# Optimization experiments

Measured on AMD Instinct MI355X. Metric: run time of the kernel, lower is better.

The kernel has to match this reference:

```python
import jax, jax.numpy as jnp
import numpy as np
import math

HIDDEN = 256
NUM_GAUSSIANS = 64
NUM_FILTERS = 256
CUTOFF = 1.0
COSINE_OFFSET = 0.0
N_NODES = 10000
N_EDGES = 320000


def ssp(x):
    # shifted softplus: softplus(x) - log(2)
    return jax.nn.softplus(x) - jnp.log(2.0).astype(x.dtype)


def setup_inputs() -> dict:
    key = jax.random.key(0)
    ks = jax.random.split(key, 12)

    def xavier(k, fan_out, fan_in):
        a = math.sqrt(6.0 / (fan_in + fan_out))
        return jax.random.uniform(k, (fan_out, fan_in), jnp.float32, -a, a)

    x = jax.random.normal(ks[0], (N_NODES, HIDDEN), jnp.float32)
    ji_pairs = jax.random.randint(ks[1], (2, N_EDGES), 0, N_NODES, jnp.int64)
    e_ji = jax.random.uniform(ks[2], (N_EDGES,), jnp.float32)  # distances in [0, cutoff)
    e_ji_basis = jax.random.normal(ks[3], (N_EDGES, NUM_GAUSSIANS), jnp.float32)

    return {
        "x": x,
        "ji_pairs": ji_pairs,
        "e_ji": e_ji,
        "e_ji_basis": e_ji_basis,
        # filter_nn: Linear(G->F), ssp, Linear(F->F)
        "fw1": xavier(ks[4], NUM_FILTERS, NUM_GAUSSIANS),
        "fb1": jnp.zeros((NUM_FILTERS,), jnp.float32),
        "fw2": xavier(ks[5], NUM_FILTERS, NUM_FILTERS),
        "fb2": jnp.zeros((NUM_FILTERS,), jnp.float32),
        # CFConv linears
        "w1": xavier(ks[6], NUM_FILTERS, HIDDEN),            # linear1, no bias
        "w2": xavier(ks[7], HIDDEN, NUM_FILTERS),            # linear2
        "b2": jnp.zeros((HIDDEN,), jnp.float32),
        # linear3
        "w3": xavier(ks[8], HIDDEN, HIDDEN),
        "b3": jnp.zeros((HIDDEN,), jnp.float32),
    }


def reference(x, ji_pairs, e_ji, e_ji_basis, fw1, fb1, fw2, fb2, w1, w2, b2, w3, b3):
    pi = jnp.asarray(math.pi, x.dtype)
    # cosine cutoff: C = 0.25 * (cos((e - off) * pi / (cutoff - off)) + 1)
    C = 0.25 * (jnp.cos((e_ji - COSINE_OFFSET) * pi / (CUTOFF - COSINE_OFFSET)) + 1.0)
    # filter network on edge RBF features: [E, F]
    W = ssp(e_ji_basis @ fw1.T + fb1) @ fw2.T + fb2
    W = W * C[:, None]
    # linear1 (no bias): [N, F]
    h = x @ w1.T
    # message: x_j * W, gathered from source nodes ji_pairs[0]
    src, dst = ji_pairs[0], ji_pairs[1]
    msg = h[src] * W                                   # [E, F]
    agg = jax.ops.segment_sum(msg, dst, num_segments=x.shape[0])  # [N, F]
    # linear2
    out = agg @ w2.T + b2
    # interaction block tail: act + linear3
    out = ssp(out) @ w3.T + b3
    return out
```

## Files before the change

### kernel.cpp

```cpp
#include <hip/hip_runtime.h>
#include <hip/hip_bf16.h>

typedef __bf16 bf16_t;
typedef float f32x4 __attribute__((ext_vector_type(4)));
typedef __bf16 bf16x8 __attribute__((ext_vector_type(8)));

#define NNODES 10000
#define NEDGES 320000
#define NPAD   10048
#define NB2    (NEDGES / 64)

#define OFF_AGG   256
#define OFF_JIN   (OFF_AGG  + (size_t)NPAD * 256 * 4)
#define OFF_HIST  (OFF_JIN  + (size_t)2 * NEDGES * 4)
#define OFF_CUR   (OFF_HIST + 10240 * 4)
#define OFF_CSR   (OFF_CUR  + 10240 * 4)
#define OFF_PERM  (OFF_CSR  + 10240 * 4)
#define OFF_SRCS  (OFF_PERM + (size_t)NEDGES * 4)
#define OFF_DSTS  (OFF_SRCS + (size_t)NEDGES * 4)
#define OFF_CES   (OFF_DSTS + (size_t)NEDGES * 4)
#define OFF_CE    (OFF_CES  + (size_t)NEDGES * 4)
#define OFF_WB    (OFF_CE   + (size_t)NEDGES * 4)
#define FW1B 0
#define FW2B 16384
#define W1B  81920
#define W2B  147456
#define W3B  212992
#define FB1B 278528
#define FB2B 278784
#define B2B  279040
#define B3B  279296
#define WBN  279552
#define WS_NEED (OFF_WB + (size_t)WBN * 2)

__device__ __forceinline__ float ssp_f(float v) {
    return fmaxf(v, 0.f) + __logf(1.f + __expf(-fabsf(v))) - 0.69314718055994531f;
}
__device__ __forceinline__ f32x4 mfma16(bf16x8 a, bf16x8 b, f32x4 c) {
    return __builtin_amdgcn_mfma_f32_16x16x32_bf16(a, b, c, 0, 0, 0);
}
template<bool ISB>
__device__ __forceinline__ bf16x8 ld8(const void* p, size_t off) {
    if constexpr (ISB) return *(const bf16x8*)((const bf16_t*)p + off);
    else {
        const float* f = (const float*)p + off;
        f32x4 lo = *(const f32x4*)f, hi = *(const f32x4*)(f + 4);
        bf16x8 r;
        for (int j = 0; j < 4; ++j) { r[j] = (bf16_t)lo[j]; r[j + 4] = (bf16_t)hi[j]; }
        return r;
    }
}
template<bool ISB>
__device__ __forceinline__ void st1(void* p, size_t off, float v) {
    if constexpr (ISB) ((bf16_t*)p)[off] = (bf16_t)v;
    else               ((float*)p)[off] = v;
}
__device__ __forceinline__ float ld1r(bool isb, const void* p, size_t off) {
    return isb ? (float)((const bf16_t*)p)[off] : ((const float*)p)[off];
}

__global__ __launch_bounds__(256) void detect_kernel(
    const void* __restrict__ x, const int* __restrict__ jraw,
    int* __restrict__ flags, int* __restrict__ hist)
{
    __shared__ int cnt, hi;
    if (threadIdx.x == 0) { cnt = 0; hi = 0; }
    __syncthreads();
    const unsigned short* xw = (const unsigned short*)x;
    int local = 0;
    for (int i = threadIdx.x; i < 2048; i += 256) {
        unsigned int e = (xw[2 * i] >> 7) & 0xFF;
        if (e >= 100 && e <= 141) local++;
    }
    atomicAdd(&cnt, local);
    int v = 0;
    for (int i = threadIdx.x; i < 1024; i += 256) v |= jraw[2 * i + 1];
    if (v != 0) atomicOr(&hi, 1);
    for (int i = threadIdx.x; i < 10240; i += 256) hist[i] = 0;
    __syncthreads();
    if (threadIdx.x == 0) { flags[0] = (cnt > 1024) ? 1 : 0; flags[1] = (hi == 0) ? 1 : 0; }
}

__global__ __launch_bounds__(256) void prep_kernel(
    const int* __restrict__ raw, const int* __restrict__ flags,
    const void* __restrict__ e_ji,
    const void* fw1, const void* fb1, const void* fw2, const void* fb2,
    const void* w1, const void* w2, const void* b2, const void* w3, const void* b3,
    int* __restrict__ jin, int* __restrict__ hist, float* __restrict__ ce,
    bf16_t* __restrict__ wb, float* __restrict__ agg)
{
    const bool is64 = (flags[1] != 0);
    const bool isb  = (flags[0] != 0);
    const int gid = blockIdx.x * 256 + threadIdx.x;
    if (gid < 2 * NEDGES) {
        int iv = is64 ? raw[2 * gid] : raw[gid];
        iv = iv < 0 ? 0 : (iv >= NNODES ? NNODES - 1 : iv);
        jin[gid] = iv;
        if (gid >= NEDGES) atomicAdd(&hist[iv], 1);
    }
    if (gid < NEDGES)
        ce[gid] = 0.25f * (cosf(3.14159265358979f * ld1r(isb, e_ji, gid)) + 1.0f);
    if (gid < WBN) {
        int g = gid; const void* s; int so;
        if      (g < FW2B) { s = fw1; so = g - FW1B; }
        else if (g < W1B)  { s = fw2; so = g - FW2B; }
        else if (g < W2B)  { s = w1;  so = g - W1B; }
        else if (g < W3B)  { s = w2;  so = g - W2B; }
        else if (g < FB1B) { s = w3;  so = g - W3B; }
        else if (g < FB2B) { s = fb1; so = g - FB1B; }
        else if (g < B2B)  { s = fb2; so = g - FB2B; }
        else if (g < B3B)  { s = b2;  so = g - B2B; }
        else               { s = b3;  so = g - B3B; }
        wb[gid] = (bf16_t)ld1r(isb, s, so);
    }
    f32x4 z = {0.f, 0.f, 0.f, 0.f};
    for (int i = gid; i < NPAD * 256 / 4; i += 2500 * 256)
        ((f32x4*)agg)[i] = z;
}

__global__ __launch_bounds__(256) void scan_kernel(
    const int* __restrict__ hist, int* __restrict__ cur, int* __restrict__ csr)
{
    __shared__ int s[256];
    const int t = threadIdx.x;
    int loc[40]; int sum = 0;
    const int base = t * 40;
    for (int j = 0; j < 40; ++j) {
        int i = base + j;
        loc[j] = (i < NNODES) ? hist[i] : 0;
        sum += loc[j];
    }
    s[t] = sum; __syncthreads();
    for (int off = 1; off < 256; off <<= 1) {
        int v = (t >= off) ? s[t - off] : 0;
        __syncthreads();
        if (t >= off) s[t] += v;
        __syncthreads();
    }
    int pre = (t == 0) ? 0 : s[t - 1];
    for (int j = 0; j < 40; ++j) {
        int i = base + j;
        cur[i] = pre;
        csr[i] = pre;
        pre += loc[j];
    }
}

__global__ __launch_bounds__(256) void scatter_kernel(
    const int* __restrict__ jin, const float* __restrict__ ce,
    int* __restrict__ cur, int* __restrict__ perm,
    int* __restrict__ src_s, int* __restrict__ dst_s, float* __restrict__ ce_s)
{
    int e = blockIdx.x * 256 + threadIdx.x;
    if (e < NEDGES) {
        int d = jin[NEDGES + e];
        int pos = atomicAdd(&cur[d], 1);
        perm[pos]  = e;
        src_s[pos] = jin[e];
        dst_s[pos] = d;
        ce_s[pos]  = ce[e];
    }
}

template<bool ISB>
__global__ __launch_bounds__(256, 2) void h_gemm_kernel(
    const void* __restrict__ x, const bf16_t* __restrict__ wb,
    bf16_t* __restrict__ h, const int* __restrict__ flags)
{
    if ((flags[0] != 0) != ISB) return;
    const bf16_t* w1b = wb + W1B;
    const int w = threadIdx.x >> 6, L = threadIdx.x & 63;
    const int lane16 = L & 15, quad = L >> 4;
    const int nb = blockIdx.x * 64, cb = w * 64;
    f32x4 acc[4][4] = {};
    for (int kc = 0; kc < 8; ++kc) {
        const int ko = kc * 32 + quad * 8;
        bf16x8 af[4], bfr[4];
        for (int mt = 0; mt < 4; ++mt) {
            int row = nb + mt * 16 + lane16;
            if (row >= NNODES) row = NNODES - 1;
            af[mt] = ld8<ISB>(x, (size_t)row * 256 + ko);
        }
        for (int nt = 0; nt < 4; ++nt)
            bfr[nt] = *(const bf16x8*)(w1b + (size_t)(cb + nt * 16 + lane16) * 256 + ko);
        for (int mt = 0; mt < 4; ++mt)
            for (int nt = 0; nt < 4; ++nt)
                acc[mt][nt] = mfma16(af[mt], bfr[nt], acc[mt][nt]);
    }
    for (int mt = 0; mt < 4; ++mt)
        for (int r = 0; r < 4; ++r) {
            int row = nb + mt * 16 + quad * 4 + r;
            if (row < NNODES)
                for (int nt = 0; nt < 4; ++nt)
                    h[(size_t)row * 256 + cb + nt * 16 + lane16] = (bf16_t)acc[mt][nt][r];
        }
}

template<bool ISB>
__global__ __launch_bounds__(256, 4) void edge_kernel2(
    const void* __restrict__ basis, const int* __restrict__ perm,
    const int* __restrict__ src_s, const int* __restrict__ dst_s,
    const float* __restrict__ ce_s,
    const bf16_t* __restrict__ wb, const bf16_t* __restrict__ h,
    float* __restrict__ agg, const int* __restrict__ flags)
{
    if ((flags[0] != 0) != ISB) return;
    __shared__ bf16_t T[64][264];
    __shared__ int sperm[64], ssrc[64], sdst[64];
    __shared__ float sce[64];
    const int tid = threadIdx.x;
    const int w = tid >> 6, L = tid & 63;
    const int lane16 = L & 15, quad = L >> 4;
    const int cb = w * 64;
    const int e0 = blockIdx.x * 64;

    {
        if      (w == 0) sperm[L] = perm[e0 + L];
        else if (w == 1) ssrc[L] = src_s[e0 + L];
        else if (w == 2) sdst[L] = dst_s[e0 + L];
        else             sce[L]  = ce_s[e0 + L];
    }

    const bf16_t* fw1b = wb + FW1B;
    const bf16_t* fw2b = wb + FW2B;
    float fb1v[4], fb2v[4];
    for (int nt = 0; nt < 4; ++nt) {
        fb1v[nt] = (float)wb[FB1B + cb + nt * 16 + lane16];
        fb2v[nt] = (float)wb[FB2B + cb + nt * 16 + lane16];
    }
    __syncthreads();

    const int hrow = tid >> 2, hseg = tid & 3;
    bf16x8 hreg[8];
    {
        const bf16_t* hs = h + (size_t)ssrc[hrow] * 256 + hseg * 64;
        #pragma unroll
        for (int j = 0; j < 8; ++j) hreg[j] = ((const bf16x8*)hs)[j];
    }

    int prow[4];
    for (int mt = 0; mt < 4; ++mt) prow[mt] = sperm[mt * 16 + lane16];

    f32x4 acc1[4][4] = {};
    for (int kc = 0; kc < 2; ++kc) {
        const int ko = kc * 32 + quad * 8;
        bf16x8 af[4], bfr[4];
        for (int mt = 0; mt < 4; ++mt)
            af[mt] = ld8<ISB>(basis, (size_t)prow[mt] * 64 + ko);
        for (int nt = 0; nt < 4; ++nt)
            bfr[nt] = *(const bf16x8*)(fw1b + (size_t)(cb + nt * 16 + lane16) * 64 + ko);
        for (int mt = 0; mt < 4; ++mt)
            for (int nt = 0; nt < 4; ++nt)
                acc1[mt][nt] = mfma16(af[mt], bfr[nt], acc1[mt][nt]);
    }
    for (int nt = 0; nt < 4; ++nt) {
        int col = cb + nt * 16 + lane16;
        for (int mt = 0; mt < 4; ++mt)
            for (int r = 0; r < 4; ++r)
                T[mt * 16 + quad * 4 + r][col] = (bf16_t)ssp_f(acc1[mt][nt][r] + fb1v[nt]);
    }
    __syncthreads();

    f32x4 acc2[4][4] = {};
    for (int kc = 0; kc < 8; ++kc) {
        const int ko = kc * 32 + quad * 8;
        bf16x8 af[4], bfr[4];
        for (int mt = 0; mt < 4; ++mt)
            af[mt] = *(const bf16x8*)(&T[mt * 16 + lane16][ko]);
        for (int nt = 0; nt < 4; ++nt)
            bfr[nt] = *(const bf16x8*)(fw2b + (size_t)(cb + nt * 16 + lane16) * 256 + ko);
        for (int mt = 0; mt < 4; ++mt)
            for (int nt = 0; nt < 4; ++nt)
                acc2[mt][nt] = mfma16(af[mt], bfr[nt], acc2[mt][nt]);
    }
    __syncthreads();

    {
        bf16_t* dp = &T[hrow][hseg * 64];
        #pragma unroll
        for (int j = 0; j < 8; ++j) ((bf16x8*)dp)[j] = hreg[j];
    }
    __syncthreads();

    float run[4] = {0, 0, 0, 0};
    int curn = -1;
    for (int mt = 0; mt < 4; ++mt)
        for (int r = 0; r < 4; ++r) {
            int row = mt * 16 + quad * 4 + r;
            int n = sdst[row];
            if (n != curn) {
                if (curn >= 0)
                    for (int nt = 0; nt < 4; ++nt)
                        atomicAdd(&agg[(size_t)curn * 256 + cb + nt * 16 + lane16], run[nt]);
                curn = n;
                run[0] = run[1] = run[2] = run[3] = 0.f;
            }
            float cv = sce[row];
            for (int nt = 0; nt < 4; ++nt) {
                int col = cb + nt * 16 + lane16;
                run[nt] += (acc2[mt][nt][r] + fb2v[nt]) * cv * (float)T[row][col];
            }
        }
    if (curn >= 0)
        for (int nt = 0; nt < 4; ++nt)
            atomicAdd(&agg[(size_t)curn * 256 + cb + nt * 16 + lane16], run[nt]);
}

template<bool ISB>
__global__ __launch_bounds__(256, 2) void out_kernel(
    const float* __restrict__ agg, const bf16_t* __restrict__ wb,
    void* __restrict__ out, const int* __restrict__ flags)
{
    if ((flags[0] != 0) != ISB) return;
    const bf16_t* w2b = wb + W2B;
    const bf16_t* w3b = wb + W3B;
    __shared__ bf16_t U[64][264];
    const int w = threadIdx.x >> 6, L = threadIdx.x & 63;
    const int lane16 = L & 15, quad = L >> 4;
    const int nb = blockIdx.x * 64, cb = w * 64;

    f32x4 acc[4][4] = {};
    for (int kc = 0; kc < 8; ++kc) {
        const int ko = kc * 32 + quad * 8;
        bf16x8 af[4], bfr[4];
        for (int mt = 0; mt < 4; ++mt) {
            int row = nb + mt * 16 + lane16;
            const float* p = agg + (size_t)row * 256 + ko;
            f32x4 lo = *(const f32x4*)p, hi = *(const f32x4*)(p + 4);
            bf16x8 a;
            for (int j = 0; j < 4; ++j) { a[j] = (bf16_t)lo[j]; a[j + 4] = (bf16_t)hi[j]; }
            af[mt] = a;
        }
        for (int nt = 0; nt < 4; ++nt)
            bfr[nt] = *(const bf16x8*)(w2b + (size_t)(cb + nt * 16 + lane16) * 256 + ko);
        for (int mt = 0; mt < 4; ++mt)
            for (int nt = 0; nt < 4; ++nt)
                acc[mt][nt] = mfma16(af[mt], bfr[nt], acc[mt][nt]);
    }
    for (int nt = 0; nt < 4; ++nt) {
        int col = cb + nt * 16 + lane16;
        float bias = (float)wb[B2B + col];
        for (int mt = 0; mt < 4; ++mt)
            for (int r = 0; r < 4; ++r)
                U[mt * 16 + quad * 4 + r][col] = (bf16_t)ssp_f(acc[mt][nt][r] + bias);
    }
    __syncthreads();

    f32x4 acc2[4][4] = {};
    for (int kc = 0; kc < 8; ++kc) {
        const int ko = kc * 32 + quad * 8;
        bf16x8 af[4], bfr[4];
        for (int mt = 0; mt < 4; ++mt)
            af[mt] = *(const bf16x8*)(&U[mt * 16 + lane16][ko]);
        for (int nt = 0; nt < 4; ++nt)
            bfr[nt] = *(const bf16x8*)(w3b + (size_t)(cb + nt * 16 + lane16) * 256 + ko);
        for (int mt = 0; mt < 4; ++mt)
            for (int nt = 0; nt < 4; ++nt)
                acc2[mt][nt] = mfma16(af[mt], bfr[nt], acc2[mt][nt]);
    }
    for (int mt = 0; mt < 4; ++mt)
        for (int r = 0; r < 4; ++r) {
            int row = nb + mt * 16 + quad * 4 + r;
            if (row < NNODES)
                for (int nt = 0; nt < 4; ++nt) {
                    int col = cb + nt * 16 + lane16;
                    st1<ISB>(out, (size_t)row * 256 + col,
                             acc2[mt][nt][r] + (float)wb[B3B + col]);
                }
        }
}

extern "C" void kernel_launch(void* const* d_in, const int* in_sizes, int n_in,
                              void* d_out, int out_size, void* d_ws, size_t ws_size,
                              hipStream_t stream) {
    const void* x     = d_in[0];
    const int*  ji    = (const int*)d_in[1];
    const void* e_ji  = d_in[2];
    const void* basis = d_in[3];
    const void* fw1   = d_in[4];
    const void* fb1   = d_in[5];
    const void* fw2   = d_in[6];
    const void* fb2   = d_in[7];
    const void* w1    = d_in[8];
    const void* w2    = d_in[9];
    const void* b2    = d_in[10];
    const void* w3    = d_in[11];
    const void* b3    = d_in[12];

    if (ws_size < WS_NEED) return;

    char* W = (char*)d_ws;
    int*    flags = (int*)W;
    float*  agg   = (float*)(W + OFF_AGG);
    int*    jin   = (int*)(W + OFF_JIN);
    int*    hist  = (int*)(W + OFF_HIST);
    int*    cur   = (int*)(W + OFF_CUR);
    int*    csr   = (int*)(W + OFF_CSR);
    int*    perm  = (int*)(W + OFF_PERM);
    int*    src_s = (int*)(W + OFF_SRCS);
    int*    dst_s = (int*)(W + OFF_DSTS);
    float*  ce_s  = (float*)(W + OFF_CES);
    float*  ce    = (float*)(W + OFF_CE);
    bf16_t* wb    = (bf16_t*)(W + OFF_WB);
    bf16_t* h     = (bf16_t*)d_out;

    detect_kernel<<<1, 256, 0, stream>>>(x, ji, flags, hist);
    prep_kernel<<<2500, 256, 0, stream>>>(ji, flags, e_ji, fw1, fb1, fw2, fb2,
                                          w1, w2, b2, w3, b3, jin, hist, ce, wb, agg);
    scan_kernel<<<1, 256, 0, stream>>>(hist, cur, csr);
    scatter_kernel<<<1250, 256, 0, stream>>>(jin, ce, cur, perm, src_s, dst_s, ce_s);
    h_gemm_kernel<true ><<<157, 256, 0, stream>>>(x, wb, h, flags);
    h_gemm_kernel<false><<<157, 256, 0, stream>>>(x, wb, h, flags);
    edge_kernel2<true ><<<NB2, 256, 0, stream>>>(basis, perm, src_s, dst_s, ce_s, wb, h, agg, flags);
    edge_kernel2<false><<<NB2, 256, 0, stream>>>(basis, perm, src_s, dst_s, ce_s, wb, h, agg, flags);
    out_kernel<true ><<<157, 256, 0, stream>>>(agg, wb, d_out, flags);
    out_kernel<false><<<157, 256, 0, stream>>>(agg, wb, d_out, flags);
}
```

Measured before the change: 525.8 us.

## Pre-reduce edge messages in shared memory before global atomics; swizzle block order

Edges are sorted by destination, so each 64-edge block usually spans only a handful of nodes (about 2 on average). The edge kernel now accumulates per-node partial sums in a small shared-memory buffer, with a fallback to direct global atomics when the span exceeds 5 nodes. It then issues one global atomic per column per node, which cuts global atomic traffic because the four quads no longer each flush separately. It also remaps block IDs so that consecutive blocks handle edge chunks far apart, presumably to reduce atomic contention on shared boundary nodes across XCDs, at the cost of LDS zeroing, an extra barrier and shared-memory atomics.

```diff
diff --git a/kernel.cpp b/kernel.cpp
--- a/kernel.cpp
+++ b/kernel.cpp
@@ -9,6 +9,7 @@
 #define NEDGES 320000
 #define NPAD   10048
 #define NB2    (NEDGES / 64)
+#define GSLOT  5
 
 #define OFF_AGG   256
 #define OFF_JIN   (OFF_AGG  + (size_t)NPAD * 256 * 4)
@@ -197,7 +198,7 @@
 }
 
 template<bool ISB>
-__global__ __launch_bounds__(256, 4) void edge_kernel2(
+__global__ __launch_bounds__(256, 4) void edge_kernel_sp(
     const void* __restrict__ basis, const int* __restrict__ perm,
     const int* __restrict__ src_s, const int* __restrict__ dst_s,
     const float* __restrict__ ce_s,
@@ -206,20 +207,21 @@
 {
     if ((flags[0] != 0) != ISB) return;
     __shared__ bf16_t T[64][264];
+    __shared__ float G[GSLOT][260];
     __shared__ int sperm[64], ssrc[64], sdst[64];
     __shared__ float sce[64];
     const int tid = threadIdx.x;
     const int w = tid >> 6, L = tid & 63;
     const int lane16 = L & 15, quad = L >> 4;
     const int cb = w * 64;
-    const int e0 = blockIdx.x * 64;
-
-    {
-        if      (w == 0) sperm[L] = perm[e0 + L];
-        else if (w == 1) ssrc[L] = src_s[e0 + L];
-        else if (w == 2) sdst[L] = dst_s[e0 + L];
-        else             sce[L]  = ce_s[e0 + L];
-    }
+    const int bid = (int)blockIdx.x;
+    const int e0 = ((bid & 7) * (NB2 / 8) + (bid >> 3)) * 64;
+
+    if      (w == 0) sperm[L] = perm[e0 + L];
+    else if (w == 1) ssrc[L] = src_s[e0 + L];
+    else if (w == 2) sdst[L] = dst_s[e0 + L];
+    else             sce[L]  = ce_s[e0 + L];
+    for (int i = tid; i < GSLOT * 260; i += 256) (&G[0][0])[i] = 0.f;
 
     const bf16_t* fw1b = wb + FW1B;
     const bf16_t* fw2b = wb + FW2B;
@@ -229,6 +231,10 @@
         fb2v[nt] = (float)wb[FB2B + cb + nt * 16 + lane16];
     }
     __syncthreads();
+
+    const int sbase = sdst[0];
+    const int span  = sdst[63] - sbase + 1;
+    const bool fbk  = (span > GSLOT);
 
     const int hrow = tid >> 2, hseg = tid & 3;
     bf16x8 hreg[8];
@@ -289,9 +295,14 @@
             int row = mt * 16 + quad * 4 + r;
             int n = sdst[row];
             if (n != curn) {
-                if (curn >= 0)
-                    for (int nt = 0; nt < 4; ++nt)
-                        atomicAdd(&agg[(size_t)curn * 256 + cb + nt * 16 + lane16], run[nt]);
+                if (curn >= 0) {
+                    if (!fbk)
+                        for (int nt = 0; nt < 4; ++nt)
+                            atomicAdd(&G[curn - sbase][cb + nt * 16 + lane16], run[nt]);
+                    else
+                        for (int nt = 0; nt < 4; ++nt)
+                            atomicAdd(&agg[(size_t)curn * 256 + cb + nt * 16 + lane16], run[nt]);
+                }
                 curn = n;
                 run[0] = run[1] = run[2] = run[3] = 0.f;
             }
@@ -301,9 +312,20 @@
                 run[nt] += (acc2[mt][nt][r] + fb2v[nt]) * cv * (float)T[row][col];
             }
         }
-    if (curn >= 0)
-        for (int nt = 0; nt < 4; ++nt)
-            atomicAdd(&agg[(size_t)curn * 256 + cb + nt * 16 + lane16], run[nt]);
+    if (curn >= 0) {
+        if (!fbk)
+            for (int nt = 0; nt < 4; ++nt)
+                atomicAdd(&G[curn - sbase][cb + nt * 16 + lane16], run[nt]);
+        else
+            for (int nt = 0; nt < 4; ++nt)
+                atomicAdd(&agg[(size_t)curn * 256 + cb + nt * 16 + lane16], run[nt]);
+    }
+    __syncthreads();
+
+    if (!fbk) {
+        for (int s = 0; s < span; ++s)
+            atomicAdd(&agg[(size_t)(sbase + s) * 256 + tid], G[s][tid]);
+    }
 }
 
 template<bool ISB>
@@ -411,8 +433,8 @@
     scatter_kernel<<<1250, 256, 0, stream>>>(jin, ce, cur, perm, src_s, dst_s, ce_s);
     h_gemm_kernel<true ><<<157, 256, 0, stream>>>(x, wb, h, flags);
     h_gemm_kernel<false><<<157, 256, 0, stream>>>(x, wb, h, flags);
-    edge_kernel2<true ><<<NB2, 256, 0, stream>>>(basis, perm, src_s, dst_s, ce_s, wb, h, agg, flags);
-    edge_kernel2<false><<<NB2, 256, 0, stream>>>(basis, perm, src_s, dst_s, ce_s, wb, h, agg, flags);
+    edge_kernel_sp<true ><<<NB2, 256, 0, stream>>>(basis, perm, src_s, dst_s, ce_s, wb, h, agg, flags);
+    edge_kernel_sp<false><<<NB2, 256, 0, stream>>>(basis, perm, src_s, dst_s, ce_s, wb, h, agg, flags);
     out_kernel<true ><<<157, 256, 0, stream>>>(agg, wb, d_out, flags);
     out_kernel<false><<<157, 256, 0, stream>>>(agg, wb, d_out, flags);
 }
```

Result: no change. 515.9 us (-1.9%).
